# Optimization experiments

Hardware: AMD Instinct MI355X
Metric: run time of the kernel (lower is better)

The kernel has to match this reference:

```python
import jax, jax.numpy as jnp
import numpy as np
import math

N, IN_DIM, Z, H, OUT, K = 16384, 64, 128, 1, 3, 16


def setup_inputs() -> dict:
    key = jax.random.key(0)
    ks = jax.random.split(key, 16)

    def lin(k, din, dout):
        kw, kb = jax.random.split(k)
        W = jax.random.normal(kw, (din, dout), jnp.float32) / math.sqrt(din)
        b = jax.random.normal(kb, (dout,), jnp.float32) * 0.01
        return W, b

    x = jax.random.normal(ks[0], (N, IN_DIM), jnp.float32)
    t = jnp.zeros((1,), jnp.float32)
    # layer dims: (in, heads*out) per TransformerConv
    dims = [(IN_DIM, Z * H), (Z * H, (Z // H) * H), (Z * H, (OUT // H) * H)]
    params = {}
    i = 1
    for li, (din, dout) in enumerate(dims, 1):
        for nm in ("q", "k", "v", "s"):
            W, b = lin(ks[i], din, dout)
            i += 1
            params[f"W{nm}{li}"] = W
            params[f"b{nm}{li}"] = b
    return {"t": t, "x": x, **params}


def knn_edge_index(coo, k):
    # kNN graph on 3-D coords (loop=False): edges neighbor(src) -> center(dst)
    n = coo.shape[0]
    sq = jnp.sum(coo * coo, axis=-1)
    d = sq[:, None] + sq[None, :] - 2.0 * (coo @ coo.T)  # [N, N] sq. distances
    d = d.at[jnp.arange(n), jnp.arange(n)].set(jnp.inf)  # exclude self-loops
    _, idx = jax.lax.top_k(-d, k)  # [N, K] nearest neighbor indices
    src = idx.reshape(-1)
    dst = jnp.repeat(jnp.arange(n), k)
    return src, dst


def tconv(x, src, dst, Wq, bq, Wk, bk, Wv, bv, Ws, bs, heads):
    # PyG TransformerConv (concat=True, root_weight=True, no edge_attr)
    n = x.shape[0]
    dout = Wq.shape[1]
    c = dout // heads
    q = (x @ Wq + bq).reshape(n, heads, c)
    kk = (x @ Wk + bk).reshape(n, heads, c)
    v = (x @ Wv + bv).reshape(n, heads, c)
    alpha = jnp.sum(q[dst] * kk[src], axis=-1) / math.sqrt(c)  # [E, H]
    amax = jax.ops.segment_max(alpha, dst, num_segments=n)
    ex = jnp.exp(alpha - amax[dst])
    denom = jax.ops.segment_sum(ex, dst, num_segments=n)
    w = ex / denom[dst]  # softmax over incoming edges per node
    msg = w[:, :, None] * v[src]  # [E, H, C]
    out = jax.ops.segment_sum(msg, dst, num_segments=n).reshape(n, dout)
    return out + x @ Ws + bs  # root/skip connection


def reference(t, x,
              Wq1, bq1, Wk1, bk1, Wv1, bv1, Ws1, bs1,
              Wq2, bq2, Wk2, bk2, Wv2, bv2, Ws2, bs2,
              Wq3, bq3, Wk3, bk3, Wv3, bv3, Ws3, bs3):
    src, dst = knn_edge_index(x[:, :3], K)  # built under no_grad in original
    h = jnp.tanh(tconv(x, src, dst, Wq1, bq1, Wk1, bk1, Wv1, bv1, Ws1, bs1, H))
    h = jnp.tanh(tconv(h, src, dst, Wq2, bq2, Wk2, bk2, Wv2, bv2, Ws2, bs2, H) + h)
    drift_coo = tconv(h, src, dst, Wq3, bq3, Wk3, bk3, Wv3, bv3, Ws3, bs3, H)
    return drift_coo
```

## Files before the change

### kernel.cpp

```cpp
#include <hip/hip_runtime.h>
#include <math.h>

#define NN 16384
#define QPW 2
#define CAP 128
#define WM 64
#define KTOP 17

typedef unsigned long long u64;

__global__ __launch_bounds__(256) void pack_coords(const float* __restrict__ x,
                                                   float4* __restrict__ coo) {
  int i = blockIdx.x * 256 + threadIdx.x;
  float a = x[i * 64 + 0];
  float b = x[i * 64 + 1];
  float c = x[i * 64 + 2];
  coo[i] = make_float4(a, b, c, a * a + b * b + c * c);
}

__device__ __forceinline__ int mbcnt64(u64 mask) {
  return __builtin_amdgcn_mbcnt_hi(
      (unsigned)(mask >> 32),
      __builtin_amdgcn_mbcnt_lo((unsigned)mask, 0));
}

__device__ __forceinline__ unsigned fmap(float d) {
  unsigned ub = __float_as_uint(d);
  return ub ^ ((unsigned)((int)ub >> 31) | 0x80000000u);
}

__device__ __forceinline__ float unfmap(unsigned ub) {
  unsigned fb = (ub & 0x80000000u) ? (ub ^ 0x80000000u) : ~ub;
  return __uint_as_float(fb);
}

__device__ __forceinline__ unsigned short f2bf(float f) {
  unsigned u = __float_as_uint(f);
  return (unsigned short)((u + 0x7FFFu + ((u >> 16) & 1u)) >> 16);
}
__device__ __forceinline__ float bf2f(unsigned short h) {
  return __uint_as_float(((unsigned)h) << 16);
}

__device__ __forceinline__ u64 u64min(u64 a, u64 b) { return a < b ? a : b; }
__device__ __forceinline__ u64 u64max(u64 a, u64 b) { return a > b ? a : b; }

__device__ __forceinline__ void sort128(u64& r0, u64& r1, int lane) {
#pragma unroll
  for (int k = 2; k <= 128; k <<= 1) {
    if (k == 128) {
      u64 lo = u64min(r0, r1);
      r1 = u64max(r0, r1);
      r0 = lo;
    }
#pragma unroll
    for (int jj = (k == 128 ? 32 : (k >> 1)); jj >= 1; jj >>= 1) {
      const bool up = (lane & jj) == 0;
      const bool asc0 = (lane & k) == 0;
      const bool asc1 = ((lane | 64) & k) == 0;
      u64 o0 = __shfl_xor(r0, jj);
      u64 o1 = __shfl_xor(r1, jj);
      r0 = (up == asc0) ? u64min(r0, o0) : u64max(r0, o0);
      r1 = (up == asc1) ? u64min(r1, o1) : u64max(r1, o1);
    }
  }
}

__device__ __forceinline__ void radix_shrink(u64* buf, int& cnt, float& th,
                                             int lane) {
  const u64 k0 = (lane < cnt) ? buf[lane] : ~0ull;
  const u64 k1 = (lane + 64 < cnt) ? buf[lane + 64] : ~0ull;
  const unsigned d0 = (unsigned)(k0 >> 32);
  const unsigned d1 = (unsigned)(k1 >> 32);
  unsigned p = 0u;
#pragma unroll
  for (int b = 31; b >= 0; --b) {
    const unsigned c = p | (1u << b);
    const u64 b0 = __ballot(d0 < c);
    const u64 b1 = __ballot(d1 < c);
    const int n = __popcll(b0) + __popcll(b1);
    if (n < KTOP) p = c;
  }
  const bool v0 = d0 <= p;
  const bool v1 = d1 <= p;
  const u64 m0 = __ballot(v0);
  const u64 m1 = __ballot(v1);
  const int base = __popcll(m0);
  if (v0) buf[mbcnt64(m0)] = k0;
  if (v1) buf[base + mbcnt64(m1)] = k1;
  cnt = base + __popcll(m1);
  th = unfmap(p);
}

__global__ __launch_bounds__(256) void knn_kernel(const float4* __restrict__ coo,
                                                  int* __restrict__ src) {
  __shared__ u64 bufs[4][QPW][CAP];
  const int lane = threadIdx.x & 63;
  const int wid = threadIdx.x >> 6;
  const int node0 = blockIdx.x * (4 * QPW) + wid * QPW;

  float nx[QPW], ny[QPW], nz[QPW], sq[QPW], th[QPW];
  int cnt[QPW];
#pragma unroll
  for (int q = 0; q < QPW; ++q) {
    const float4 me = coo[node0 + q];
    nx[q] = -2.0f * me.x;
    ny[q] = -2.0f * me.y;
    nz[q] = -2.0f * me.z;
    sq[q] = me.w;
    cnt[q] = 0;
  }

  {
    const float4 pa = coo[lane];
    const float4 pb = coo[64 + lane];
#pragma unroll
    for (int q = 0; q < QPW; ++q) {
      const float d0 = sq[q] + fmaf(nx[q], pa.x,
                           fmaf(ny[q], pa.y, fmaf(nz[q], pa.z, pa.w)));
      const float d1 = sq[q] + fmaf(nx[q], pb.x,
                           fmaf(ny[q], pb.y, fmaf(nz[q], pb.z, pb.w)));
      bufs[wid][q][lane] = ((u64)fmap(d0) << 32) | (unsigned)lane;
      bufs[wid][q][64 + lane] = ((u64)fmap(d1) << 32) | (unsigned)(64 + lane);
      cnt[q] = 128;
      radix_shrink(bufs[wid][q], cnt[q], th[q], lane);
    }
  }

  float4 s0 = coo[2 * 64 + lane];
  float4 s1 = coo[3 * 64 + lane];
  float4 s2 = coo[4 * 64 + lane];
  float4 s3 = coo[5 * 64 + lane];

  auto body = [&](const float4 cur, const int step) {
    const int j = step * 64 + lane;
    float dd[QPW];
#pragma unroll
    for (int q = 0; q < QPW; ++q)
      dd[q] = sq[q] + fmaf(nx[q], cur.x,
                           fmaf(ny[q], cur.y, fmaf(nz[q], cur.z, cur.w)));
    u64 mk[QPW];
#pragma unroll
    for (int q = 0; q < QPW; ++q) mk[q] = __ballot(dd[q] <= th[q]);
    if (mk[0] | mk[1]) {
#pragma unroll
      for (int q = 0; q < QPW; ++q) {
        if (mk[q]) {
          if (dd[q] <= th[q])
            bufs[wid][q][cnt[q] + mbcnt64(mk[q])] =
                ((u64)fmap(dd[q]) << 32) | (unsigned)j;
          cnt[q] += __popcll(mk[q]);
          if (cnt[q] >= WM) radix_shrink(bufs[wid][q], cnt[q], th[q], lane);
        }
      }
    }
  };

#pragma unroll 1
  for (int g = 0; g < 63; ++g) {
    const int base = 2 + g * 4;
    body(s0, base + 0);
    s0 = coo[(base + 4) * 64 + lane];
    body(s1, base + 1);
    s1 = coo[(base + 5) * 64 + lane];
    body(s2, base + 2);
    s2 = coo[(base + 6) * 64 + lane];
    body(s3, base + 3);
    s3 = coo[(base + 7) * 64 + lane];
  }
  body(s0, 254);
  body(s1, 255);

#pragma unroll 1
  for (int q = 0; q < QPW; ++q) {
    u64 r0 = (lane < cnt[q]) ? bufs[wid][q][lane] : ~0ull;
    u64 r1 = (lane + 64 < cnt[q]) ? bufs[wid][q][lane + 64] : ~0ull;
    sort128(r0, r1, lane);
    const int idx = (int)(r0 & 0xFFFFFFFFull);
    const u64 selfm = __ballot((lane < KTOP) && (idx == node0 + q));
    const int s = selfm ? (__ffsll((long long)selfm) - 1) : 99;
    const int outrank = lane - (lane > s ? 1 : 0);
    if (lane < KTOP && lane != s && outrank < 16)
      src[(node0 + q) * 16 + outrank] = idx;
  }
}

template <int KD>
__global__ __launch_bounds__(256) void gemm_qkvs(
    const float* __restrict__ X, const float* __restrict__ W0,
    const float* __restrict__ W1, const float* __restrict__ W2,
    const float* __restrict__ W3, const float* __restrict__ B0,
    const float* __restrict__ B1, const float* __restrict__ B2,
    const float* __restrict__ B3, float* __restrict__ qs,
    unsigned short* __restrict__ kvh) {
  __shared__ float As[64][68];
  __shared__ float Bs[64][64];
  const int brow = blockIdx.x * 64;
  const int by = blockIdx.y;
  const int wi = by >> 1;
  const float* W = wi == 0 ? W0 : wi == 1 ? W1 : wi == 2 ? W2 : W3;
  const float* bias = wi == 0 ? B0 : wi == 1 ? B1 : wi == 2 ? B2 : B3;
  const int cbase = (by & 1) * 64;
  const int tx = threadIdx.x & 15;
  const int ty = threadIdx.x >> 4;

  float acc[4][4] = {};
  for (int k0 = 0; k0 < KD; k0 += 64) {
    __syncthreads();
#pragma unroll
    for (int i = 0; i < 4; ++i) {
      const int flat = threadIdx.x * 4 + i * 1024;
      const int r = flat >> 6, kk = flat & 63;
      const float4 v = *(const float4*)&X[(brow + r) * KD + k0 + kk];
      As[kk + 0][r] = v.x;
      As[kk + 1][r] = v.y;
      As[kk + 2][r] = v.z;
      As[kk + 3][r] = v.w;
    }
#pragma unroll
    for (int i = 0; i < 4; ++i) {
      const int flat = threadIdx.x * 4 + i * 1024;
      const int kk = flat >> 6, c = flat & 63;
      *(float4*)&Bs[kk][c] = *(const float4*)&W[(k0 + kk) * 128 + cbase + c];
    }
    __syncthreads();
#pragma unroll 8
    for (int k = 0; k < 64; ++k) {
      const float4 a = *(const float4*)&As[k][ty * 4];
      const float4 b = *(const float4*)&Bs[k][tx * 4];
      const float av[4] = {a.x, a.y, a.z, a.w};
      const float bv[4] = {b.x, b.y, b.z, b.w};
#pragma unroll
      for (int i = 0; i < 4; ++i)
#pragma unroll
        for (int jj = 0; jj < 4; ++jj)
          acc[i][jj] = fmaf(av[i], bv[jj], acc[i][jj]);
    }
  }
  const float4 bi = *(const float4*)&bias[cbase + tx * 4];
  const int col = cbase + tx * 4;
#pragma unroll
  for (int i = 0; i < 4; ++i) {
    const int row = brow + ty * 4 + i;
    float4 o;
    o.x = acc[i][0] + bi.x;
    o.y = acc[i][1] + bi.y;
    o.z = acc[i][2] + bi.z;
    o.w = acc[i][3] + bi.w;
    if (wi == 0) {
      *(float4*)&qs[row * 256 + col] = o;
    } else if (wi == 3) {
      *(float4*)&qs[row * 256 + 128 + col] = o;
    } else {
      ushort4 h;
      h.x = f2bf(o.x);
      h.y = f2bf(o.y);
      h.z = f2bf(o.z);
      h.w = f2bf(o.w);
      *(ushort4*)&kvh[row * 256 + (wi == 1 ? col : 128 + col)] = h;
    }
  }
}

__global__ __launch_bounds__(256) void attn_c128(
    const float* __restrict__ qs, const unsigned short* __restrict__ kvh,
    const int* __restrict__ src, const float* __restrict__ res,
    float* __restrict__ hout, int do_res) {
  const int g = threadIdx.x >> 5;
  const int node = blockIdx.x * 8 + g;
  const int c = threadIdx.x & 31;
  const float4 q4 = ((const float4*)(qs + node * 256))[c];

  int nb[16];
#pragma unroll
  for (int r = 0; r < 16; ++r) nb[r] = src[node * 16 + r];

  float p[16];
#pragma unroll
  for (int r = 0; r < 16; ++r) {
    const ushort4 k4 = ((const ushort4*)(kvh + nb[r] * 256))[c];
    p[r] = q4.x * bf2f(k4.x) + q4.y * bf2f(k4.y) + q4.z * bf2f(k4.z) +
           q4.w * bf2f(k4.w);
  }
#pragma unroll
  for (int o = 16; o; o >>= 1) {
#pragma unroll
    for (int r = 0; r < 16; ++r) p[r] += __shfl_xor(p[r], o);
  }

  float m = p[0];
#pragma unroll
  for (int r = 1; r < 16; ++r) m = fmaxf(m, p[r]);
  float w[16];
  float den = 0.0f;
#pragma unroll
  for (int r = 0; r < 16; ++r) {
    w[r] = __expf((p[r] - m) * 0.088388347648318447f);
    den += w[r];
  }
  const float inv = 1.0f / den;
  float o0 = 0.0f, o1 = 0.0f, o2 = 0.0f, o3 = 0.0f;
#pragma unroll
  for (int r = 0; r < 16; ++r) {
    const ushort4 v4 = ((const ushort4*)(kvh + nb[r] * 256 + 128))[c];
    const float ww = w[r] * inv;
    o0 = fmaf(ww, bf2f(v4.x), o0);
    o1 = fmaf(ww, bf2f(v4.y), o1);
    o2 = fmaf(ww, bf2f(v4.z), o2);
    o3 = fmaf(ww, bf2f(v4.w), o3);
  }
  const float4 s4 = ((const float4*)(qs + node * 256 + 128))[c];
  float r0 = o0 + s4.x, r1 = o1 + s4.y, r2 = o2 + s4.z, r3 = o3 + s4.w;
  if (do_res) {
    const float4 h4 = ((const float4*)(res + node * 128))[c];
    r0 += h4.x;
    r1 += h4.y;
    r2 += h4.z;
    r3 += h4.w;
  }
  ((float4*)(hout + node * 128))[c] =
      make_float4(tanhf(r0), tanhf(r1), tanhf(r2), tanhf(r3));
}

__global__ __launch_bounds__(256) void gemm_qkvs3(
    const float* __restrict__ H, const float* __restrict__ W0,
    const float* __restrict__ W1, const float* __restrict__ W2,
    const float* __restrict__ W3, const float* __restrict__ B0,
    const float* __restrict__ B1, const float* __restrict__ B2,
    const float* __restrict__ B3, float* __restrict__ out) {
  __shared__ float hs[64][132];
  __shared__ float wsh[128 * 12];
  __shared__ float bsh[12];
  const int brow = blockIdx.x * 64;
  if (threadIdx.x < 12) {
    const int mi = threadIdx.x / 3, c = threadIdx.x % 3;
    const float* Bsel = mi == 0 ? B0 : mi == 1 ? B1 : mi == 2 ? B2 : B3;
    bsh[threadIdx.x] = Bsel[c];
  }
  for (int t = threadIdx.x; t < 1536; t += 256) {
    const int k = t / 12, cc = t % 12;
    const int mi = cc / 3, c = cc % 3;
    const float* Wsel = mi == 0 ? W0 : mi == 1 ? W1 : mi == 2 ? W2 : W3;
    wsh[t] = Wsel[k * 3 + c];
  }
#pragma unroll
  for (int i = 0; i < 8; ++i) {
    const int flat = threadIdx.x * 4 + i * 1024;
    const int r = flat >> 7, kk = flat & 127;
    *(float4*)&hs[r][kk] = *(const float4*)&H[(brow + r) * 128 + kk];
  }
  __syncthreads();
  const int r = threadIdx.x >> 2;
  const int part = threadIdx.x & 3;
  float a0 = 0.0f, a1 = 0.0f, a2 = 0.0f;
#pragma unroll 4
  for (int k = 0; k < 128; ++k) {
    const float h = hs[r][k];
    a0 = fmaf(h, wsh[k * 12 + part * 3 + 0], a0);
    a1 = fmaf(h, wsh[k * 12 + part * 3 + 1], a1);
    a2 = fmaf(h, wsh[k * 12 + part * 3 + 2], a2);
  }
  const int row = brow + r;
  out[row * 12 + part * 3 + 0] = a0 + bsh[part * 3 + 0];
  out[row * 12 + part * 3 + 1] = a1 + bsh[part * 3 + 1];
  out[row * 12 + part * 3 + 2] = a2 + bsh[part * 3 + 2];
}

__global__ __launch_bounds__(256) void attn_c3(const float* __restrict__ q3,
                                               const int* __restrict__ src,
                                               float* __restrict__ out) {
  const int gid = blockIdx.x * 256 + threadIdx.x;
  const int node = gid >> 4, r = gid & 15;
  const int j = src[node * 16 + r];
  const float* qn = q3 + node * 12;
  const float* kj = q3 + j * 12 + 3;
  float alpha = (qn[0] * kj[0] + qn[1] * kj[1] + qn[2] * kj[2]) *
                0.57735026918962576f;
  float m = alpha;
#pragma unroll
  for (int o = 8; o; o >>= 1) m = fmaxf(m, __shfl_xor(m, o, 16));
  const float e = __expf(alpha - m);
  float den = e;
#pragma unroll
  for (int o = 8; o; o >>= 1) den += __shfl_xor(den, o, 16);
  const float wgt = e / den;
  const float* vj = q3 + j * 12 + 6;
  float o0 = wgt * vj[0], o1 = wgt * vj[1], o2 = wgt * vj[2];
#pragma unroll
  for (int o = 8; o; o >>= 1) {
    o0 += __shfl_xor(o0, o, 16);
    o1 += __shfl_xor(o1, o, 16);
    o2 += __shfl_xor(o2, o, 16);
  }
  if (r == 0) {
    const float* sn = q3 + node * 12 + 9;
    out[node * 3 + 0] = o0 + sn[0];
    out[node * 3 + 1] = o1 + sn[1];
    out[node * 3 + 2] = o2 + sn[2];
  }
}

extern "C" void kernel_launch(void* const* d_in, const int* in_sizes, int n_in,
                              void* d_out, int out_size, void* d_ws,
                              size_t ws_size, hipStream_t stream) {
  const float* x = (const float*)d_in[1];
  const float* Wq1 = (const float*)d_in[2];
  const float* bq1 = (const float*)d_in[3];
  const float* Wk1 = (const float*)d_in[4];
  const float* bk1 = (const float*)d_in[5];
  const float* Wv1 = (const float*)d_in[6];
  const float* bv1 = (const float*)d_in[7];
  const float* Ws1 = (const float*)d_in[8];
  const float* bs1 = (const float*)d_in[9];
  const float* Wq2 = (const float*)d_in[10];
  const float* bq2 = (const float*)d_in[11];
  const float* Wk2 = (const float*)d_in[12];
  const float* bk2 = (const float*)d_in[13];
  const float* Wv2 = (const float*)d_in[14];
  const float* bv2 = (const float*)d_in[15];
  const float* Ws2 = (const float*)d_in[16];
  const float* bs2 = (const float*)d_in[17];
  const float* Wq3 = (const float*)d_in[18];
  const float* bq3 = (const float*)d_in[19];
  const float* Wk3 = (const float*)d_in[20];
  const float* bk3 = (const float*)d_in[21];
  const float* Wv3 = (const float*)d_in[22];
  const float* bv3 = (const float*)d_in[23];
  const float* Ws3 = (const float*)d_in[24];
  const float* bs3 = (const float*)d_in[25];

  const size_t MB = 1024 * 1024;
  char* ws = (char*)d_ws;
  float* qs = (float*)(ws);
  unsigned short* kvh = (unsigned short*)(ws + 16 * MB);
  float* h1 = (float*)(ws + 24 * MB);
  float* h2 = (float*)(ws + 32 * MB);
  int* src = (int*)(ws + 40 * MB);
  float4* coo = (float4*)(ws + 41 * MB);
  float* q3 = (float*)(ws + 42 * MB);
  float* out = (float*)d_out;

  pack_coords<<<NN / 256, 256, 0, stream>>>(x, coo);
  knn_kernel<<<NN / (4 * QPW), 256, 0, stream>>>(coo, src);
  gemm_qkvs<64><<<dim3(NN / 64, 8), 256, 0, stream>>>(
      x, Wq1, Wk1, Wv1, Ws1, bq1, bk1, bv1, bs1, qs, kvh);
  attn_c128<<<NN / 8, 256, 0, stream>>>(qs, kvh, src, nullptr, h1, 0);
  gemm_qkvs<128><<<dim3(NN / 64, 8), 256, 0, stream>>>(
      h1, Wq2, Wk2, Wv2, Ws2, bq2, bk2, bv2, bs2, qs, kvh);
  attn_c128<<<NN / 8, 256, 0, stream>>>(qs, kvh, src, h1, h2, 1);
  gemm_qkvs3<<<NN / 64, 256, 0, stream>>>(h2, Wq3, Wk3, Wv3, Ws3, bq3, bk3,
                                          bv3, bs3, q3);
  attn_c3<<<NN * 16 / 256, 256, 0, stream>>>(q3, src, out);
}
```

Baseline: 301.9 us.

## Pack kNN coords in paired SoA layout and use packed-FP32 distance math

Coordinates are repacked so each lane loads two candidates' x/y/z/|p|^2 as float2 pairs, letting the kNN scan compute two distances per instruction with packed FMA. The comparison is rewritten as a 'larger is closer' score (dot minus half norm), which drops the per-query norm add. Each step now handles 128 candidates, with a larger candidate buffer and a 4-way radix shrink for overflow, and the final sort is reduced to 64 elements after a last shrink. This targets the ALU cost of the dominant distance scan, but it doubles shared memory per block and adds more branching in the insert path.

```diff
diff --git a/kernel.cpp b/kernel.cpp
--- a/kernel.cpp
+++ b/kernel.cpp
@@ -3,19 +3,26 @@
 
 #define NN 16384
 #define QPW 2
-#define CAP 128
+#define CAP 256
 #define WM 64
 #define KTOP 17
 
 typedef unsigned long long u64;
+typedef float v2f __attribute__((ext_vector_type(2)));
+typedef float f4v __attribute__((ext_vector_type(4)));
 
 __global__ __launch_bounds__(256) void pack_coords(const float* __restrict__ x,
-                                                   float4* __restrict__ coo) {
+                                                   float* __restrict__ pc) {
   int i = blockIdx.x * 256 + threadIdx.x;
   float a = x[i * 64 + 0];
   float b = x[i * 64 + 1];
   float c = x[i * 64 + 2];
-  coo[i] = make_float4(a, b, c, a * a + b * b + c * c);
+  const int m = (i >> 7) * 64 + (i & 63);
+  const int h = (i >> 6) & 1;
+  pc[m * 8 + 0 + h] = a;
+  pc[m * 8 + 2 + h] = b;
+  pc[m * 8 + 4 + h] = c;
+  pc[m * 8 + 6 + h] = a * a + b * b + c * c;
 }
 
 __device__ __forceinline__ int mbcnt64(u64 mask) {
@@ -45,29 +52,21 @@
 __device__ __forceinline__ u64 u64min(u64 a, u64 b) { return a < b ? a : b; }
 __device__ __forceinline__ u64 u64max(u64 a, u64 b) { return a > b ? a : b; }
 
-__device__ __forceinline__ void sort128(u64& r0, u64& r1, int lane) {
-#pragma unroll
-  for (int k = 2; k <= 128; k <<= 1) {
-    if (k == 128) {
-      u64 lo = u64min(r0, r1);
-      r1 = u64max(r0, r1);
-      r0 = lo;
-    }
-#pragma unroll
-    for (int jj = (k == 128 ? 32 : (k >> 1)); jj >= 1; jj >>= 1) {
+__device__ __forceinline__ void sort64(u64& r0, int lane) {
+#pragma unroll
+  for (int k = 2; k <= 64; k <<= 1) {
+#pragma unroll
+    for (int jj = k >> 1; jj >= 1; jj >>= 1) {
       const bool up = (lane & jj) == 0;
-      const bool asc0 = (lane & k) == 0;
-      const bool asc1 = ((lane | 64) & k) == 0;
-      u64 o0 = __shfl_xor(r0, jj);
-      u64 o1 = __shfl_xor(r1, jj);
-      r0 = (up == asc0) ? u64min(r0, o0) : u64max(r0, o0);
-      r1 = (up == asc1) ? u64min(r1, o1) : u64max(r1, o1);
-    }
-  }
-}
-
-__device__ __forceinline__ void radix_shrink(u64* buf, int& cnt, float& th,
-                                             int lane) {
+      const bool asc = (lane & k) == 0;
+      u64 o = __shfl_xor(r0, jj);
+      r0 = (up == asc) ? u64min(r0, o) : u64max(r0, o);
+    }
+  }
+}
+
+__device__ __forceinline__ void radix_shrink2(u64* buf, int& cnt, float& th,
+                                              int lane) {
   const u64 k0 = (lane < cnt) ? buf[lane] : ~0ull;
   const u64 k1 = (lane + 64 < cnt) ? buf[lane + 64] : ~0ull;
   const unsigned d0 = (unsigned)(k0 >> 32);
@@ -92,90 +91,138 @@
   th = unfmap(p);
 }
 
-__global__ __launch_bounds__(256) void knn_kernel(const float4* __restrict__ coo,
+__device__ __forceinline__ void radix_shrink4(u64* buf, int& cnt, float& th,
+                                              int lane) {
+  u64 k[4];
+  unsigned d[4];
+#pragma unroll
+  for (int i = 0; i < 4; ++i) {
+    k[i] = (lane + i * 64 < cnt) ? buf[lane + i * 64] : ~0ull;
+    d[i] = (unsigned)(k[i] >> 32);
+  }
+  unsigned p = 0u;
+#pragma unroll
+  for (int b = 31; b >= 0; --b) {
+    const unsigned c = p | (1u << b);
+    int n = 0;
+#pragma unroll
+    for (int i = 0; i < 4; ++i) n += __popcll(__ballot(d[i] < c));
+    if (n < KTOP) p = c;
+  }
+  int base = 0;
+#pragma unroll
+  for (int i = 0; i < 4; ++i) {
+    const bool v = d[i] <= p;
+    const u64 m = __ballot(v);
+    if (v) buf[base + mbcnt64(m)] = k[i];
+    base += __popcll(m);
+  }
+  cnt = base;
+  th = unfmap(p);
+}
+
+__global__ __launch_bounds__(256) void knn_kernel(const float* __restrict__ pc,
                                                   int* __restrict__ src) {
   __shared__ u64 bufs[4][QPW][CAP];
   const int lane = threadIdx.x & 63;
   const int wid = threadIdx.x >> 6;
   const int node0 = blockIdx.x * (4 * QPW) + wid * QPW;
-
-  float nx[QPW], ny[QPW], nz[QPW], sq[QPW], th[QPW];
+  const f4v* pc4 = (const f4v*)pc;
+
+  v2f qxv[QPW], qyv[QPW], qzv[QPW];
+  float th[QPW], cq[QPW];
   int cnt[QPW];
 #pragma unroll
   for (int q = 0; q < QPW; ++q) {
-    const float4 me = coo[node0 + q];
-    nx[q] = -2.0f * me.x;
-    ny[q] = -2.0f * me.y;
-    nz[q] = -2.0f * me.z;
-    sq[q] = me.w;
+    const int n = node0 + q;
+    const int mq = (n >> 7) * 64 + (n & 63);
+    const int hq = (n >> 6) & 1;
+    const float qx = pc[mq * 8 + 0 + hq];
+    const float qy = pc[mq * 8 + 2 + hq];
+    const float qz = pc[mq * 8 + 4 + hq];
+    qxv[q] = (v2f){qx, qx};
+    qyv[q] = (v2f){qy, qy};
+    qzv[q] = (v2f){qz, qz};
     cnt[q] = 0;
-  }
-
-  {
-    const float4 pa = coo[lane];
-    const float4 pb = coo[64 + lane];
+    cq[q] = -INFINITY;
+  }
+
+  auto body = [&](const f4v A, const f4v B, const int step) {
+    const int j0 = step * 128 + lane;
+    const v2f X = __builtin_shufflevector(A, A, 0, 1);
+    const v2f Y = __builtin_shufflevector(A, A, 2, 3);
+    const v2f Z = __builtin_shufflevector(B, B, 0, 1);
+    const v2f W = __builtin_shufflevector(B, B, 2, 3);
+    const v2f T = W * -0.5f;
+    v2f L[QPW];
+#pragma unroll
+    for (int q = 0; q < QPW; ++q)
+      L[q] = __builtin_elementwise_fma(
+          qxv[q], X,
+          __builtin_elementwise_fma(
+              qyv[q], Y, __builtin_elementwise_fma(qzv[q], Z, T)));
 #pragma unroll
     for (int q = 0; q < QPW; ++q) {
-      const float d0 = sq[q] + fmaf(nx[q], pa.x,
-                           fmaf(ny[q], pa.y, fmaf(nz[q], pa.z, pa.w)));
-      const float d1 = sq[q] + fmaf(nx[q], pb.x,
-                           fmaf(ny[q], pb.y, fmaf(nz[q], pb.z, pb.w)));
-      bufs[wid][q][lane] = ((u64)fmap(d0) << 32) | (unsigned)lane;
-      bufs[wid][q][64 + lane] = ((u64)fmap(d1) << 32) | (unsigned)(64 + lane);
-      cnt[q] = 128;
-      radix_shrink(bufs[wid][q], cnt[q], th[q], lane);
-    }
-  }
-
-  float4 s0 = coo[2 * 64 + lane];
-  float4 s1 = coo[3 * 64 + lane];
-  float4 s2 = coo[4 * 64 + lane];
-  float4 s3 = coo[5 * 64 + lane];
-
-  auto body = [&](const float4 cur, const int step) {
-    const int j = step * 64 + lane;
-    float dd[QPW];
-#pragma unroll
-    for (int q = 0; q < QPW; ++q)
-      dd[q] = sq[q] + fmaf(nx[q], cur.x,
-                           fmaf(ny[q], cur.y, fmaf(nz[q], cur.z, cur.w)));
-    u64 mk[QPW];
-#pragma unroll
-    for (int q = 0; q < QPW; ++q) mk[q] = __ballot(dd[q] <= th[q]);
-    if (mk[0] | mk[1]) {
-#pragma unroll
-      for (int q = 0; q < QPW; ++q) {
-        if (mk[q]) {
-          if (dd[q] <= th[q])
-            bufs[wid][q][cnt[q] + mbcnt64(mk[q])] =
-                ((u64)fmap(dd[q]) << 32) | (unsigned)j;
-          cnt[q] += __popcll(mk[q]);
-          if (cnt[q] >= WM) radix_shrink(bufs[wid][q], cnt[q], th[q], lane);
+      const u64 ma = __ballot(L[q].x >= cq[q]);
+      const u64 mb = __ballot(L[q].y >= cq[q]);
+      if (ma | mb) {
+        const int pa = __popcll(ma);
+        if (L[q].x >= cq[q])
+          bufs[wid][q][cnt[q] + mbcnt64(ma)] =
+              (((u64)fmap(-L[q].x)) << 32) | (unsigned)j0;
+        if (L[q].y >= cq[q])
+          bufs[wid][q][cnt[q] + pa + mbcnt64(mb)] =
+              (((u64)fmap(-L[q].y)) << 32) | (unsigned)(j0 + 64);
+        cnt[q] += pa + __popcll(mb);
+        if (cnt[q] >= WM) {
+          if (cnt[q] <= 128)
+            radix_shrink2(bufs[wid][q], cnt[q], th[q], lane);
+          else
+            radix_shrink4(bufs[wid][q], cnt[q], th[q], lane);
+          cq[q] = -th[q];
         }
       }
     }
   };
 
+  {
+    const f4v A = pc4[lane * 2 + 0];
+    const f4v B = pc4[lane * 2 + 1];
+    body(A, B, 0);
+  }
+
+  f4v s0A = pc4[1 * 128 + lane * 2 + 0], s0B = pc4[1 * 128 + lane * 2 + 1];
+  f4v s1A = pc4[2 * 128 + lane * 2 + 0], s1B = pc4[2 * 128 + lane * 2 + 1];
+  f4v s2A = pc4[3 * 128 + lane * 2 + 0], s2B = pc4[3 * 128 + lane * 2 + 1];
+  f4v s3A = pc4[4 * 128 + lane * 2 + 0], s3B = pc4[4 * 128 + lane * 2 + 1];
+
 #pragma unroll 1
-  for (int g = 0; g < 63; ++g) {
-    const int base = 2 + g * 4;
-    body(s0, base + 0);
-    s0 = coo[(base + 4) * 64 + lane];
-    body(s1, base + 1);
-    s1 = coo[(base + 5) * 64 + lane];
-    body(s2, base + 2);
-    s2 = coo[(base + 6) * 64 + lane];
-    body(s3, base + 3);
-    s3 = coo[(base + 7) * 64 + lane];
-  }
-  body(s0, 254);
-  body(s1, 255);
+  for (int g = 0; g < 31; ++g) {
+    const int base = 1 + g * 4;
+    body(s0A, s0B, base + 0);
+    s0A = pc4[(base + 4) * 128 + lane * 2 + 0];
+    s0B = pc4[(base + 4) * 128 + lane * 2 + 1];
+    body(s1A, s1B, base + 1);
+    s1A = pc4[(base + 5) * 128 + lane * 2 + 0];
+    s1B = pc4[(base + 5) * 128 + lane * 2 + 1];
+    body(s2A, s2B, base + 2);
+    s2A = pc4[(base + 6) * 128 + lane * 2 + 0];
+    s2B = pc4[(base + 6) * 128 + lane * 2 + 1];
+    body(s3A, s3B, base + 3);
+    s3A = pc4[(base + 7) * 128 + lane * 2 + 0];
+    s3B = pc4[(base + 7) * 128 + lane * 2 + 1];
+  }
+  body(s0A, s0B, 125);
+  body(s1A, s1B, 126);
+  body(s2A, s2B, 127);
 
 #pragma unroll 1
   for (int q = 0; q < QPW; ++q) {
+    if (cnt[q] > 64) {
+      radix_shrink2(bufs[wid][q], cnt[q], th[q], lane);
+    }
     u64 r0 = (lane < cnt[q]) ? bufs[wid][q][lane] : ~0ull;
-    u64 r1 = (lane + 64 < cnt[q]) ? bufs[wid][q][lane + 64] : ~0ull;
-    sort128(r0, r1, lane);
+    sort64(r0, lane);
     const int idx = (int)(r0 & 0xFFFFFFFFull);
     const u64 selfm = __ballot((lane < KTOP) && (idx == node0 + q));
     const int s = selfm ? (__ffsll((long long)selfm) - 1) : 99;
@@ -436,12 +483,12 @@
   float* h1 = (float*)(ws + 24 * MB);
   float* h2 = (float*)(ws + 32 * MB);
   int* src = (int*)(ws + 40 * MB);
-  float4* coo = (float4*)(ws + 41 * MB);
+  float* pc = (float*)(ws + 41 * MB);
   float* q3 = (float*)(ws + 42 * MB);
   float* out = (float*)d_out;
 
-  pack_coords<<<NN / 256, 256, 0, stream>>>(x, coo);
-  knn_kernel<<<NN / (4 * QPW), 256, 0, stream>>>(coo, src);
+  pack_coords<<<NN / 256, 256, 0, stream>>>(x, pc);
+  knn_kernel<<<NN / (4 * QPW), 256, 0, stream>>>(pc, src);
   gemm_qkvs<64><<<dim3(NN / 64, 8), 256, 0, stream>>>(
       x, Wq1, Wk1, Wv1, Ws1, bq1, bk1, bv1, bs1, qs, kvh);
   attn_c128<<<NN / 8, 256, 0, stream>>>(qs, kvh, src, nullptr, h1, 0);
```

Measured after the change: 317.3 us. 5.1% more time.
